# Kernel tuning notes

Measured on AMD Instinct MI355X. Metric: run time of the kernel, lower is better.

Reference implementation:

```python
import jax, jax.numpy as jnp
import numpy as np

# Static config matching init_kwargs
WZ, WH, WW = 2, 6, 12          # window size
MZ, MH, MW = 4, 16, 15          # ceil(input_shape / window_size) for (8,96,180)
HEADS, DIM, B = 6, 192, 1
DH = DIM // HEADS
P = WZ * WH * WW                # 144 tokens per window
WN = MZ * MH * MW               # 960 windows
WT = MZ * MH                    # 64 window types
SCALE = DH ** -0.5
TABLE = WZ * WZ * WH * WH * (2 * WW - 1)  # 3312 bias entries


def _position_index():
    zi = np.arange(WZ); zj = -np.arange(WZ) * WZ
    hi = np.arange(WH); hj = -np.arange(WH) * WH
    w = np.arange(WW)
    c1 = np.stack(np.meshgrid(zi, hi, w, indexing='ij')).reshape(3, -1)  # (3, P)
    c2 = np.stack(np.meshgrid(zj, hj, w, indexing='ij')).reshape(3, -1)  # (3, P)
    coords = (c1[:, :, None] - c2[:, None, :]).transpose(1, 2, 0)        # (P, P, 3)
    coords[:, :, 2] += WW - 1
    coords[:, :, 1] *= 2 * WW - 1
    coords[:, :, 0] *= (2 * WW - 1) * WH * WH
    return coords.sum(-1).reshape(-1)  # (P*P,)

POS_IDX = jnp.asarray(_position_index())


def setup_inputs() -> dict:
    key = jax.random.key(0)
    ks = jax.random.split(key, 5)
    x = jax.random.normal(ks[0], (B * WN, P, DIM), dtype=jnp.float32)
    mask = jnp.zeros((WN, P, P), dtype=jnp.float32)
    w_qkv = jax.random.normal(ks[1], (DIM, 3 * DIM), dtype=jnp.float32) * 0.02
    w_proj = jax.random.normal(ks[2], (DIM, DIM), dtype=jnp.float32) * 0.02
    b_proj = jnp.zeros((DIM,), dtype=jnp.float32)
    bias_table = jax.random.normal(ks[3], (TABLE, WT, HEADS), dtype=jnp.float32) * 0.02
    return {"x": x, "mask": mask, "w_qkv": w_qkv, "w_proj": w_proj,
            "b_proj": b_proj, "bias_table": bias_table}


def reference(x, mask, w_qkv, w_proj, b_proj, bias_table):
    BN = x.shape[0]  # B*WN
    qkv = (x @ w_qkv).reshape(BN, P, 3, HEADS, DH).transpose(2, 0, 3, 1, 4)  # (3,BN,h,P,dh)
    q, k, v = SCALE * qkv[0], qkv[1], qkv[2]
    attn = jnp.einsum('bhid,bhjd->bhij', q, k)  # (BN, h, P, P)
    # (B mZ mH mW) h P P -> (B mW) (mZ mH) h P P
    attn = attn.reshape(B, MZ, MH, MW, HEADS, P, P)
    attn = attn.transpose(0, 3, 1, 2, 4, 5, 6).reshape(B * MW, WT, HEADS, P, P)
    # gather earth-specific bias: (P*P, WT, h) -> (WT, h, P, P)
    bias = bias_table[POS_IDX].reshape(P, P, WT, HEADS).transpose(2, 3, 0, 1)
    attn = attn + bias  # broadcast over (B mW)
    # back to (B mZ mH mW) h P P
    attn = attn.reshape(B, MW, MZ, MH, HEADS, P, P)
    attn = attn.transpose(0, 2, 3, 1, 4, 5, 6).reshape(B, WN, HEADS, P, P)
    attn = attn + mask[None, :, None]  # (1, wN, 1, P, P)
    attn = jax.nn.softmax(attn, axis=-1).reshape(B * WN, HEADS, P, P)
    out = jnp.einsum('bhij,bhjd->bhid', attn, v)           # (BN, h, P, dh)
    out = out.transpose(0, 2, 1, 3).reshape(BN, P, DIM)    # merge heads
    return out @ w_proj + b_proj
```

## Files before the change

kernel.cpp:

```cpp
#include <hip/hip_runtime.h>

#define HEADS 6
#define DIM 192
#define DH 32
#define PW 144
#define WN 960
#define MWD 15
#define NTOK (WN*PW)
#define SCALE 0.17677669529663687f

typedef __attribute__((ext_vector_type(8))) short bf16x8;
typedef __attribute__((ext_vector_type(4))) short bf16x4;
typedef __attribute__((ext_vector_type(4))) float f32x4;

#define MFMA16(a,b,c) __builtin_amdgcn_mfma_f32_16x16x32_bf16(a,b,c,0,0,0)

__device__ __forceinline__ unsigned short f2bf(float f) {
    unsigned int u = __builtin_bit_cast(unsigned int, f);
    u += 0x7fffu + ((u >> 16) & 1u);
    return (unsigned short)(u >> 16);
}
__device__ __forceinline__ float bf2f(unsigned short s) {
    unsigned int u = ((unsigned int)s) << 16;
    return __builtin_bit_cast(float, u);
}

__global__ void prep_weights(const float* __restrict__ wqkv,
                             const float* __restrict__ wproj,
                             unsigned short* __restrict__ wqkvT,
                             unsigned short* __restrict__ wprojT) {
    int t = blockIdx.x * 256 + threadIdx.x;
    if (t < 576 * 192) {
        int n = t / 192, k = t % 192;
        wqkvT[t] = f2bf(wqkv[k * 576 + n]);
    } else {
        int t2 = t - 576 * 192;
        int n = t2 / 192, k = t2 % 192;
        wprojT[t2] = f2bf(wproj[k * 192 + n]);
    }
}

__global__ void prep_bias(const float* __restrict__ table,
                          unsigned short* __restrict__ bias_d) {
    int t = blockIdx.x * 256 + threadIdx.x;
    int j = t % 144;
    int i = (t / 144) % 144;
    int h = (t / 20736) % 6;
    int wt = t / 124416;
    int z1 = i / 72, h1 = (i / 12) % 6, w1 = i % 12;
    int z2 = j / 72, h2 = (j / 12) % 6, w2 = j % 12;
    int pos = (z1 + 2 * z2) * 828 + (h1 + 6 * h2) * 23 + (w1 - w2 + 11);
    bias_d[t] = f2bf(table[pos * 384 + wt * 6 + h]);
}

__global__ __launch_bounds__(256) void prep_cast(const float* __restrict__ x,
                                                 unsigned short* __restrict__ xb) {
    long long c = (long long)blockIdx.x * 256 + threadIdx.x;
    const float* p = x + c * 8;
    f32x4 v0 = *(const f32x4*)p;
    f32x4 v1 = *(const f32x4*)(p + 4);
    bf16x8 o;
    o[0] = (short)f2bf(v0[0]); o[1] = (short)f2bf(v0[1]);
    o[2] = (short)f2bf(v0[2]); o[3] = (short)f2bf(v0[3]);
    o[4] = (short)f2bf(v1[0]); o[5] = (short)f2bf(v1[1]);
    o[6] = (short)f2bf(v1[2]); o[7] = (short)f2bf(v1[3]);
    *(bf16x8*)(xb + c * 8) = o;
}

__global__ __launch_bounds__(256) void qkv_gemm(
        const unsigned short* __restrict__ xb, const unsigned short* __restrict__ wqkvT,
        unsigned short* __restrict__ qb, unsigned short* __restrict__ kb,
        unsigned short* __restrict__ vtb) {
    __shared__ unsigned short A[64 * 200];
    __shared__ unsigned short Bt[96 * 200];
    int bid = blockIdx.x;
    int r8 = bid & 7, s = bid >> 3;
    int nblk = s % 6;
    int mtile = r8 * 270 + s / 6;
    int tid = threadIdx.x;

    const unsigned short* xp = xb + (long long)mtile * (64 * 192);
    #pragma unroll
    for (int it = 0; it < 6; ++it) {
        int c = tid + it * 256;
        int row = c / 24, c8 = (c % 24) * 8;
        *(bf16x8*)&A[row * 200 + c8] = *(const bf16x8*)(xp + c * 8);
    }
    const unsigned short* wp = wqkvT + nblk * (96 * 192);
    #pragma unroll
    for (int it = 0; it < 9; ++it) {
        int c = tid + it * 256;
        int row = c / 24, c8 = (c % 24) * 8;
        *(bf16x8*)&Bt[row * 200 + c8] = *(const bf16x8*)(wp + c * 8);
    }
    __syncthreads();

    int lane = tid & 63, wv = tid >> 6;
    int l16 = lane & 15, quad = lane >> 4;
    f32x4 acc[6];
    #pragma unroll
    for (int i = 0; i < 6; ++i) acc[i] = (f32x4){0.f, 0.f, 0.f, 0.f};

    #pragma unroll
    for (int kc = 0; kc < 6; ++kc) {
        bf16x8 af = *(const bf16x8*)&A[(wv * 16 + l16) * 200 + kc * 32 + quad * 8];
        #pragma unroll
        for (int ct = 0; ct < 6; ++ct) {
            bf16x8 bfr = *(const bf16x8*)&Bt[(ct * 16 + l16) * 200 + kc * 32 + quad * 8];
            acc[ct] = MFMA16(af, bfr, acc[ct]);
        }
    }

    int token0 = mtile * 64 + wv * 16 + quad * 4;
    int win = token0 / 144;
    int p0 = token0 - win * 144;
    #pragma unroll
    for (int ct = 0; ct < 6; ++ct) {
        int c0 = nblk * 96 + ct * 16;
        int which = c0 / 192;
        int head = (c0 % 192) / 32;
        int d = (c0 % 32) + l16;
        if (which == 0) {
            int base = ((win * 6 + head) * 144 + p0) * 32 + d;
            #pragma unroll
            for (int r = 0; r < 4; ++r) qb[base + r * 32] = f2bf(acc[ct][r]);
        } else if (which == 1) {
            int base = ((win * 6 + head) * 144 + p0) * 32 + d;
            #pragma unroll
            for (int r = 0; r < 4; ++r) kb[base + r * 32] = f2bf(acc[ct][r]);
        } else {
            int base = ((win * 6 + head) * 32 + d) * 144 + p0;
            bf16x4 o;
            #pragma unroll
            for (int r = 0; r < 4; ++r) o[r] = (short)f2bf(acc[ct][r]);
            *(bf16x4*)&vtb[base] = o;
        }
    }
}

__global__ __launch_bounds__(192) void attn(
        const unsigned short* __restrict__ qb, const unsigned short* __restrict__ kb,
        const unsigned short* __restrict__ vtb, const unsigned short* __restrict__ bias_d,
        const float* __restrict__ mask, unsigned short* __restrict__ Ob) {
    __shared__ unsigned short Q[144 * 40];
    __shared__ unsigned short Kl[144 * 40];
    __shared__ unsigned short Vt[32 * 160];
    __shared__ unsigned short Pl[3 * 16 * 168];

    int bx = blockIdx.x;
    int r8 = bx & 7, s = bx >> 3;
    int h = s % 6;
    int win = r8 * 120 + s / 6;
    int wt = win / MWD;
    int tid = threadIdx.x;
    int lane = tid & 63, wv = tid >> 6;
    int l16 = lane & 15, quad = lane >> 4;

    int qoff = (win * 6 + h) * (144 * 32);
    #pragma unroll
    for (int it = 0; it < 3; ++it) {
        int c = tid + it * 192;
        int row = c >> 2, c8 = (c & 3) * 8;
        *(bf16x8*)&Q[row * 40 + c8]  = *(const bf16x8*)(qb + qoff + c * 8);
        *(bf16x8*)&Kl[row * 40 + c8] = *(const bf16x8*)(kb + qoff + c * 8);
        int vr = c / 18, vc = (c % 18) * 8;
        *(bf16x8*)&Vt[vr * 160 + vc] = *(const bf16x8*)(vtb + qoff + c * 8);
    }
    {
        int row = lane >> 2, ch = lane & 3;
        *(bf16x4*)&Pl[wv * 2688 + row * 168 + 144 + ch * 4] = (bf16x4){0, 0, 0, 0};
    }
    if (tid < 64) {
        int row = tid >> 1, off = 144 + (tid & 1) * 8;
        *(bf16x8*)&Vt[row * 160 + off] = (bf16x8){0, 0, 0, 0, 0, 0, 0, 0};
    }
    __syncthreads();

    const float* maskp = mask + win * 20736;
    const unsigned short* biasp = bias_d + (wt * 6 + h) * 20736;
    const f32x4 z = {0.f, 0.f, 0.f, 0.f};

    for (int rt = 0; rt < 3; ++rt) {
        int i0 = (wv * 3 + rt) * 16;
        bf16x8 aq = *(const bf16x8*)&Q[(i0 + l16) * 40 + quad * 8];
        f32x4 sreg[9];
        #pragma unroll
        for (int ct = 0; ct < 9; ++ct) {
            bf16x8 bk = *(const bf16x8*)&Kl[(ct * 16 + l16) * 40 + quad * 8];
            sreg[ct] = MFMA16(aq, bk, z);
        }
        #pragma unroll
        for (int ct = 0; ct < 9; ++ct) {
            int j = ct * 16 + l16;
            #pragma unroll
            for (int r = 0; r < 4; ++r) {
                int i = i0 + quad * 4 + r;
                float b = bf2f(biasp[i * 144 + j]);
                float mk = maskp[i * 144 + j];
                sreg[ct][r] = sreg[ct][r] * SCALE + b + mk;
            }
        }
        #pragma unroll
        for (int r = 0; r < 4; ++r) {
            float mx = sreg[0][r];
            #pragma unroll
            for (int ct = 1; ct < 9; ++ct) mx = fmaxf(mx, sreg[ct][r]);
            #pragma unroll
            for (int off = 1; off < 16; off <<= 1) mx = fmaxf(mx, __shfl_xor(mx, off, 64));
            float sum = 0.f;
            #pragma unroll
            for (int ct = 0; ct < 9; ++ct) { float e = __expf(sreg[ct][r] - mx); sreg[ct][r] = e; sum += e; }
            #pragma unroll
            for (int off = 1; off < 16; off <<= 1) sum += __shfl_xor(sum, off, 64);
            float inv = 1.0f / sum;
            #pragma unroll
            for (int ct = 0; ct < 9; ++ct) sreg[ct][r] *= inv;
        }
        int pb = wv * 2688;
        #pragma unroll
        for (int ct = 0; ct < 9; ++ct) {
            #pragma unroll
            for (int r = 0; r < 4; ++r)
                Pl[pb + (quad * 4 + r) * 168 + ct * 16 + l16] = f2bf(sreg[ct][r]);
        }
        f32x4 o0 = z, o1 = z;
        #pragma unroll
        for (int kc = 0; kc < 5; ++kc) {
            bf16x8 ap = *(const bf16x8*)&Pl[pb + l16 * 168 + kc * 32 + quad * 8];
            bf16x8 b0 = *(const bf16x8*)&Vt[l16 * 160 + kc * 32 + quad * 8];
            bf16x8 b1 = *(const bf16x8*)&Vt[(16 + l16) * 160 + kc * 32 + quad * 8];
            o0 = MFMA16(ap, b0, o0);
            o1 = MFMA16(ap, b1, o1);
        }
        #pragma unroll
        for (int r = 0; r < 4; ++r) {
            int i = i0 + quad * 4 + r;
            int ob = (win * 144 + i) * 192 + h * 32 + l16;
            Ob[ob] = f2bf(o0[r]);
            Ob[ob + 16] = f2bf(o1[r]);
        }
    }
}

__global__ __launch_bounds__(256) void out_gemm(
        const unsigned short* __restrict__ Ob, const unsigned short* __restrict__ wprojT,
        const float* __restrict__ bproj, float* __restrict__ out) {
    __shared__ unsigned short A[64 * 200];
    __shared__ unsigned short Bt[96 * 200];
    int bid = blockIdx.x;
    int r8 = bid & 7, s = bid >> 3;
    int nblk = s % 2;
    int mtile = r8 * 270 + s / 2;
    int tid = threadIdx.x;

    const unsigned short* op = Ob + (long long)mtile * (64 * 192);
    #pragma unroll
    for (int it = 0; it < 6; ++it) {
        int c = tid + it * 256;
        int row = c / 24, c8 = (c % 24) * 8;
        *(bf16x8*)&A[row * 200 + c8] = *(const bf16x8*)(op + c * 8);
    }
    const unsigned short* wp = wprojT + nblk * (96 * 192);
    #pragma unroll
    for (int it = 0; it < 9; ++it) {
        int c = tid + it * 256;
        int row = c / 24, c8 = (c % 24) * 8;
        *(bf16x8*)&Bt[row * 200 + c8] = *(const bf16x8*)(wp + c * 8);
    }
    __syncthreads();

    int lane = tid & 63, wv = tid >> 6;
    int l16 = lane & 15, quad = lane >> 4;
    f32x4 acc[6];
    #pragma unroll
    for (int i = 0; i < 6; ++i) acc[i] = (f32x4){0.f, 0.f, 0.f, 0.f};
    #pragma unroll
    for (int kc = 0; kc < 6; ++kc) {
        bf16x8 af = *(const bf16x8*)&A[(wv * 16 + l16) * 200 + kc * 32 + quad * 8];
        #pragma unroll
        for (int ct = 0; ct < 6; ++ct) {
            bf16x8 bfr = *(const bf16x8*)&Bt[(ct * 16 + l16) * 200 + kc * 32 + quad * 8];
            acc[ct] = MFMA16(af, bfr, acc[ct]);
        }
    }
    int token0 = mtile * 64 + wv * 16 + quad * 4;
    #pragma unroll
    for (int ct = 0; ct < 6; ++ct) {
        int c = nblk * 96 + ct * 16 + l16;
        float bp = bproj[c];
        #pragma unroll
        for (int r = 0; r < 4; ++r)
            out[(token0 + r) * 192 + c] = acc[ct][r] + bp;
    }
}

extern "C" void kernel_launch(void* const* d_in, const int* in_sizes, int n_in,
                              void* d_out, int out_size, void* d_ws, size_t ws_size,
                              hipStream_t stream) {
    const float* x     = (const float*)d_in[0];
    const float* mask  = (const float*)d_in[1];
    const float* wqkv  = (const float*)d_in[2];
    const float* wproj = (const float*)d_in[3];
    const float* bproj = (const float*)d_in[4];
    const float* btab  = (const float*)d_in[5];
    float* out = (float*)d_out;

    char* ws = (char*)d_ws;
    unsigned short* xb     = (unsigned short*)(ws + 0);
    unsigned short* Ob     = (unsigned short*)(ws + 0);
    unsigned short* qb     = (unsigned short*)(ws + 53084160);
    unsigned short* kb     = (unsigned short*)(ws + 106168320);
    unsigned short* vtb    = (unsigned short*)(ws + 159252480);
    unsigned short* bias_d = (unsigned short*)(ws + 212336640);
    unsigned short* wqkvT  = (unsigned short*)(ws + 228261888);
    unsigned short* wprojT = (unsigned short*)(ws + 228483072);

    prep_weights<<<576, 256, 0, stream>>>(wqkv, wproj, wqkvT, wprojT);
    prep_bias<<<31104, 256, 0, stream>>>(btab, bias_d);
    prep_cast<<<12960, 256, 0, stream>>>(x, xb);
    qkv_gemm<<<12960, 256, 0, stream>>>(xb, wqkvT, qb, kb, vtb);
    attn<<<5760, 192, 0, stream>>>(qb, kb, vtb, bias_d, mask, Ob);
    out_gemm<<<4320, 256, 0, stream>>>(Ob, wprojT, bproj, out);
}
```

Measured before the change: 483.4 us.

## Fuse input cast into QKV GEMM and streamline attention softmax

Removes the separate fp32-to-bf16 cast kernel by converting x while loading the A tile in the QKV GEMM. In attention, Q fragments go to registers instead of LDS, and bias plus mask are loaded ahead of the MFMAs. Softmax uses exp2 with log2e folded into the scale and bias table, and the normalization is deferred to the output. V LDS rows are padded, and an occupancy hint is added. The GEMM now rereads fp32 x once per N block, which increases global read traffic.

New measurement: 519.7 us. 1.08x slower.

```diff
diff --git a/kernel.cpp b/kernel.cpp
--- a/kernel.cpp
+++ b/kernel.cpp
@@ -8,6 +8,8 @@
 #define MWD 15
 #define NTOK (WN*PW)
 #define SCALE 0.17677669529663687f
+#define LOG2E 1.4426950408889634f
+#define SCALE2 (SCALE * LOG2E)
 
 typedef __attribute__((ext_vector_type(8))) short bf16x8;
 typedef __attribute__((ext_vector_type(4))) short bf16x4;
@@ -50,25 +52,11 @@
     int z1 = i / 72, h1 = (i / 12) % 6, w1 = i % 12;
     int z2 = j / 72, h2 = (j / 12) % 6, w2 = j % 12;
     int pos = (z1 + 2 * z2) * 828 + (h1 + 6 * h2) * 23 + (w1 - w2 + 11);
-    bias_d[t] = f2bf(table[pos * 384 + wt * 6 + h]);
-}
-
-__global__ __launch_bounds__(256) void prep_cast(const float* __restrict__ x,
-                                                 unsigned short* __restrict__ xb) {
-    long long c = (long long)blockIdx.x * 256 + threadIdx.x;
-    const float* p = x + c * 8;
-    f32x4 v0 = *(const f32x4*)p;
-    f32x4 v1 = *(const f32x4*)(p + 4);
-    bf16x8 o;
-    o[0] = (short)f2bf(v0[0]); o[1] = (short)f2bf(v0[1]);
-    o[2] = (short)f2bf(v0[2]); o[3] = (short)f2bf(v0[3]);
-    o[4] = (short)f2bf(v1[0]); o[5] = (short)f2bf(v1[1]);
-    o[6] = (short)f2bf(v1[2]); o[7] = (short)f2bf(v1[3]);
-    *(bf16x8*)(xb + c * 8) = o;
+    bias_d[t] = f2bf(table[pos * 384 + wt * 6 + h] * LOG2E);
 }
 
 __global__ __launch_bounds__(256) void qkv_gemm(
-        const unsigned short* __restrict__ xb, const unsigned short* __restrict__ wqkvT,
+        const float* __restrict__ x, const unsigned short* __restrict__ wqkvT,
         unsigned short* __restrict__ qb, unsigned short* __restrict__ kb,
         unsigned short* __restrict__ vtb) {
     __shared__ unsigned short A[64 * 200];
@@ -79,12 +67,20 @@
     int mtile = r8 * 270 + s / 6;
     int tid = threadIdx.x;
 
-    const unsigned short* xp = xb + (long long)mtile * (64 * 192);
+    const float* xp = x + (long long)mtile * (64 * 192);
     #pragma unroll
     for (int it = 0; it < 6; ++it) {
         int c = tid + it * 256;
         int row = c / 24, c8 = (c % 24) * 8;
-        *(bf16x8*)&A[row * 200 + c8] = *(const bf16x8*)(xp + c * 8);
+        const float* p = xp + c * 8;
+        f32x4 v0 = *(const f32x4*)p;
+        f32x4 v1 = *(const f32x4*)(p + 4);
+        bf16x8 o;
+        o[0] = (short)f2bf(v0[0]); o[1] = (short)f2bf(v0[1]);
+        o[2] = (short)f2bf(v0[2]); o[3] = (short)f2bf(v0[3]);
+        o[4] = (short)f2bf(v1[0]); o[5] = (short)f2bf(v1[1]);
+        o[6] = (short)f2bf(v1[2]); o[7] = (short)f2bf(v1[3]);
+        *(bf16x8*)&A[row * 200 + c8] = o;
     }
     const unsigned short* wp = wqkvT + nblk * (96 * 192);
     #pragma unroll
@@ -138,13 +134,12 @@
     }
 }
 
-__global__ __launch_bounds__(192) void attn(
+__global__ __launch_bounds__(192, 3) void attn(
         const unsigned short* __restrict__ qb, const unsigned short* __restrict__ kb,
         const unsigned short* __restrict__ vtb, const unsigned short* __restrict__ bias_d,
         const float* __restrict__ mask, unsigned short* __restrict__ Ob) {
-    __shared__ unsigned short Q[144 * 40];
     __shared__ unsigned short Kl[144 * 40];
-    __shared__ unsigned short Vt[32 * 160];
+    __shared__ unsigned short Vt[32 * 168];
     __shared__ unsigned short Pl[3 * 16 * 168];
 
     int bx = blockIdx.x;
@@ -161,28 +156,43 @@
     for (int it = 0; it < 3; ++it) {
         int c = tid + it * 192;
         int row = c >> 2, c8 = (c & 3) * 8;
-        *(bf16x8*)&Q[row * 40 + c8]  = *(const bf16x8*)(qb + qoff + c * 8);
         *(bf16x8*)&Kl[row * 40 + c8] = *(const bf16x8*)(kb + qoff + c * 8);
         int vr = c / 18, vc = (c % 18) * 8;
-        *(bf16x8*)&Vt[vr * 160 + vc] = *(const bf16x8*)(vtb + qoff + c * 8);
-    }
+        *(bf16x8*)&Vt[vr * 168 + vc] = *(const bf16x8*)(vtb + qoff + c * 8);
+    }
+    bf16x8 qreg[3];
+    #pragma unroll
+    for (int rt = 0; rt < 3; ++rt)
+        qreg[rt] = *(const bf16x8*)(qb + qoff + (((wv * 3 + rt) * 16) + l16) * 32 + quad * 8);
     {
         int row = lane >> 2, ch = lane & 3;
         *(bf16x4*)&Pl[wv * 2688 + row * 168 + 144 + ch * 4] = (bf16x4){0, 0, 0, 0};
     }
-    if (tid < 64) {
-        int row = tid >> 1, off = 144 + (tid & 1) * 8;
-        *(bf16x8*)&Vt[row * 160 + off] = (bf16x8){0, 0, 0, 0, 0, 0, 0, 0};
+    if (tid < 96) {
+        int row = tid / 3, off = 144 + (tid % 3) * 8;
+        *(bf16x8*)&Vt[row * 168 + off] = (bf16x8){0, 0, 0, 0, 0, 0, 0, 0};
     }
     __syncthreads();
 
     const float* maskp = mask + win * 20736;
     const unsigned short* biasp = bias_d + (wt * 6 + h) * 20736;
     const f32x4 z = {0.f, 0.f, 0.f, 0.f};
-
+    int pb = wv * 2688;
+
+    #pragma unroll
     for (int rt = 0; rt < 3; ++rt) {
         int i0 = (wv * 3 + rt) * 16;
-        bf16x8 aq = *(const bf16x8*)&Q[(i0 + l16) * 40 + quad * 8];
+        int ibase = (i0 + quad * 4) * 144 + l16;
+        f32x4 bm[9];
+        #pragma unroll
+        for (int ct = 0; ct < 9; ++ct) {
+            #pragma unroll
+            for (int r = 0; r < 4; ++r) {
+                int off = ibase + r * 144 + ct * 16;
+                bm[ct][r] = fmaf(maskp[off], LOG2E, bf2f(biasp[off]));
+            }
+        }
+        bf16x8 aq = qreg[rt];
         f32x4 sreg[9];
         #pragma unroll
         for (int ct = 0; ct < 9; ++ct) {
@@ -191,15 +201,11 @@
         }
         #pragma unroll
         for (int ct = 0; ct < 9; ++ct) {
-            int j = ct * 16 + l16;
-            #pragma unroll
-            for (int r = 0; r < 4; ++r) {
-                int i = i0 + quad * 4 + r;
-                float b = bf2f(biasp[i * 144 + j]);
-                float mk = maskp[i * 144 + j];
-                sreg[ct][r] = sreg[ct][r] * SCALE + b + mk;
-            }
-        }
+            #pragma unroll
+            for (int r = 0; r < 4; ++r)
+                sreg[ct][r] = fmaf(sreg[ct][r], SCALE2, bm[ct][r]);
+        }
+        float inv[4];
         #pragma unroll
         for (int r = 0; r < 4; ++r) {
             float mx = sreg[0][r];
@@ -209,14 +215,14 @@
             for (int off = 1; off < 16; off <<= 1) mx = fmaxf(mx, __shfl_xor(mx, off, 64));
             float sum = 0.f;
             #pragma unroll
-            for (int ct = 0; ct < 9; ++ct) { float e = __expf(sreg[ct][r] - mx); sreg[ct][r] = e; sum += e; }
+            for (int ct = 0; ct < 9; ++ct) {
+                float e = __builtin_amdgcn_exp2f(sreg[ct][r] - mx);
+                sreg[ct][r] = e; sum += e;
+            }
             #pragma unroll
             for (int off = 1; off < 16; off <<= 1) sum += __shfl_xor(sum, off, 64);
-            float inv = 1.0f / sum;
-            #pragma unroll
-            for (int ct = 0; ct < 9; ++ct) sreg[ct][r] *= inv;
-        }
-        int pb = wv * 2688;
+            inv[r] = __builtin_amdgcn_rcpf(sum);
+        }
         #pragma unroll
         for (int ct = 0; ct < 9; ++ct) {
             #pragma unroll
@@ -227,8 +233,8 @@
         #pragma unroll
         for (int kc = 0; kc < 5; ++kc) {
             bf16x8 ap = *(const bf16x8*)&Pl[pb + l16 * 168 + kc * 32 + quad * 8];
-            bf16x8 b0 = *(const bf16x8*)&Vt[l16 * 160 + kc * 32 + quad * 8];
-            bf16x8 b1 = *(const bf16x8*)&Vt[(16 + l16) * 160 + kc * 32 + quad * 8];
+            bf16x8 b0 = *(const bf16x8*)&Vt[l16 * 168 + kc * 32 + quad * 8];
+            bf16x8 b1 = *(const bf16x8*)&Vt[(16 + l16) * 168 + kc * 32 + quad * 8];
             o0 = MFMA16(ap, b0, o0);
             o1 = MFMA16(ap, b1, o1);
         }
@@ -236,8 +242,8 @@
         for (int r = 0; r < 4; ++r) {
             int i = i0 + quad * 4 + r;
             int ob = (win * 144 + i) * 192 + h * 32 + l16;
-            Ob[ob] = f2bf(o0[r]);
-            Ob[ob + 16] = f2bf(o1[r]);
+            Ob[ob] = f2bf(o0[r] * inv[r]);
+            Ob[ob + 16] = f2bf(o1[r] * inv[r]);
         }
     }
 }
@@ -306,7 +312,6 @@
     float* out = (float*)d_out;
 
     char* ws = (char*)d_ws;
-    unsigned short* xb     = (unsigned short*)(ws + 0);
     unsigned short* Ob     = (unsigned short*)(ws + 0);
     unsigned short* qb     = (unsigned short*)(ws + 53084160);
     unsigned short* kb     = (unsigned short*)(ws + 106168320);
@@ -317,8 +322,7 @@
 
     prep_weights<<<576, 256, 0, stream>>>(wqkv, wproj, wqkvT, wprojT);
     prep_bias<<<31104, 256, 0, stream>>>(btab, bias_d);
-    prep_cast<<<12960, 256, 0, stream>>>(x, xb);
-    qkv_gemm<<<12960, 256, 0, stream>>>(xb, wqkvT, qb, kb, vtb);
+    qkv_gemm<<<12960, 256, 0, stream>>>(x, wqkvT, qb, kb, vtb);
     attn<<<5760, 192, 0, stream>>>(qb, kb, vtb, bias_d, mask, Ob);
     out_gemm<<<4320, 256, 0, stream>>>(Ob, wprojT, bproj, out);
 }
```
